# Kernel optimization log

Measured on AMD Instinct MI355X. Metric: run time of the kernel, lower is better.

The kernel has to match this reference:

```python
import jax, jax.numpy as jnp
import numpy as np

K = 4                 # max_block_size (depthwise conv kernel size)
BLOCKS = (1, 2, 3, 4) # block sizes, offset 0
DS = 4                # downsample_factor
BLOCK_MULT = 12       # lcm(1,2,3,4)
DIM = 512
NUM_TOKENS = 256


def setup_inputs() -> dict:
    key = jax.random.key(0)
    ks = jax.random.split(key, 8)
    b, n = 4, 4096
    s = 0.02
    return {
        "x": jax.random.randint(ks[0], (b, n), 0, NUM_TOKENS),
        "emb": jax.random.normal(ks[1], (NUM_TOKENS, DIM), dtype=jnp.float32) * s,
        "conv_w": jax.random.normal(ks[2], (DIM, K), dtype=jnp.float32) * s,   # depthwise Conv1d weight [d,1,K] squeezed
        "conv_b": jax.random.normal(ks[3], (DIM,), dtype=jnp.float32) * s,
        "proj_w": jax.random.normal(ks[4], (DIM, DIM), dtype=jnp.float32) * s,  # 1x1 conv == linear [out,in]
        "proj_b": jax.random.normal(ks[5], (DIM,), dtype=jnp.float32) * s,
        "score_w": jax.random.normal(ks[6], (DIM,), dtype=jnp.float32) * s,     # nn.Linear(dim,1)
        "score_b": jax.random.normal(ks[7], (), dtype=jnp.float32) * s,
    }


def reference(x, emb, conv_w, conv_b, proj_w, proj_b, score_w, score_b):
    b, n = x.shape
    h = emb[x]  # [b, n, d] token embedding (gather)

    # pos_conv: pad (K-1) at sequence end, depthwise conv (valid), then pointwise proj
    hp = jnp.pad(h, ((0, 0), (0, K - 1), (0, 0)))
    y = conv_b + sum(hp[:, k:k + n, :] * conv_w[:, k] for k in range(K))  # [b, n, d]
    h = y @ proj_w.T + proj_b

    # pad sequence to multiple of lcm of block sizes
    L = -(-n // BLOCK_MULT) * BLOCK_MULT
    h = jnp.pad(h, ((0, 0), (0, L - n), (0, 0)))

    # multi-scale block mean pooling, upsampled back to length L
    reprs = []
    for bs in BLOCKS:
        r = h.reshape(b, L // bs, bs, DIM).mean(axis=2)     # [b, L/bs, d]
        reprs.append(jnp.repeat(r, bs, axis=1))             # [b, L, d]
    block_reprs = jnp.stack(reprs, axis=2)                  # [b, L, nb, d]

    # per-position block scores
    scores = block_reprs @ score_w + score_b                # [b, L, nb]
    scores = jax.nn.softmax(scores, axis=2)

    # consensus attention over positions (d = nb = len(BLOCKS))
    sim = jnp.einsum('bid,bjd->bij', scores, scores)        # [b, L, L]
    attn = jax.nn.softmax(sim, axis=-1)
    scores = jnp.einsum('bij,bjm->bim', attn, scores)       # [b, L, nb]

    # fuse block representations and downsample
    out = jnp.einsum('bnkd,bnk->bnd', block_reprs, scores)  # [b, L, d]
    m = -(-n // DS) * DS                                    # == n (4096 divisible by 4)
    out = out[:, :m].reshape(b, m // DS, DS, DIM).mean(axis=2)
    return out
```

## Files before the change

### kernel.cpp

```cpp
#include <hip/hip_runtime.h>
#include <hip/hip_bf16.h>

#define B_ 4
#define N_ 4096
#define L_ 4104
#define D_ 512
#define BK 64
#define NF 210
#define ZCH 36
#define ZCHUNKS 114

typedef __attribute__((ext_vector_type(8))) short bf16x8;
typedef __attribute__((ext_vector_type(4))) float f32x4;

__global__ __launch_bounds__(256) void k_g(const float* __restrict__ emb,
    const float* __restrict__ pw, const float* __restrict__ cwp,
    const float* __restrict__ cb, const float* __restrict__ pb,
    const float* __restrict__ sw,
    float* __restrict__ G, float* __restrict__ biasp,
    unsigned* __restrict__ featPk, float* __restrict__ featCf,
    float* __restrict__ Zg, float* __restrict__ TS, float* __restrict__ c0g) {
  __shared__ __align__(16) __hip_bfloat16 As[2][64 * BK];
  __shared__ __align__(16) __hip_bfloat16 Bs[2][128 * BK];
  __shared__ __align__(16) float cwS[512];
  __shared__ float red[4];
  __shared__ __align__(16) float swS[512];
  __shared__ __align__(16) float uS[512];
  __shared__ __align__(16) float vkS[512];
  const int bx = blockIdx.x;
  const int t = threadIdx.x;
  const int w = t >> 6, l = t & 63;

  if (bx >= 129) {
    const int kp = bx - 129;
    swS[t] = sw[t]; swS[t + 256] = sw[t + 256];
    __syncthreads();
    const int c2 = t * 2;
    float ux0 = 0.f, uy0 = 0.f, ux1 = 0.f, uy1 = 0.f;
#pragma unroll 4
    for (int o = 0; o < 512; o += 2) {
      const float s0 = swS[o], s1 = swS[o + 1];
      const float2 w0 = *(const float2*)(pw + (size_t)o * 512 + c2);
      const float2 w1 = *(const float2*)(pw + (size_t)(o + 1) * 512 + c2);
      ux0 += s0 * w0.x; uy0 += s0 * w0.y;
      ux1 += s1 * w1.x; uy1 += s1 * w1.y;
    }
    const float ux = ux0 + ux1, uy = uy0 + uy1;
    uS[c2] = ux; uS[c2 + 1] = uy;
    vkS[c2]     = ux * cwp[c2 * 4 + kp];
    vkS[c2 + 1] = uy * cwp[(c2 + 1) * 4 + kp];
    __syncthreads();
    const int r16 = t & 15, tg = t >> 4;
    for (int tok0 = 0; tok0 < 256; tok0 += 16) {
      const int tok = tok0 + tg;
      float dot = 0.f;
#pragma unroll
      for (int it = 0; it < 8; ++it) {
        const int c = it * 64 + r16 * 4;
        const float4 e4 = *(const float4*)(emb + (size_t)tok * 512 + c);
        const float4 v4 = *(const float4*)(vkS + c);
        dot += e4.x * v4.x + e4.y * v4.y + e4.z * v4.z + e4.w * v4.w;
      }
#pragma unroll
      for (int m = 8; m >= 1; m >>= 1) dot += __shfl_xor(dot, m);
      if (r16 == 0) TS[kp * 256 + tok] = dot;
    }
    if (kp == 0) {
      float part = cb[c2] * uS[c2] + cb[c2 + 1] * uS[c2 + 1]
                 + pb[c2] * swS[c2] + pb[c2 + 1] * swS[c2 + 1];
#pragma unroll
      for (int m = 32; m >= 1; m >>= 1) part += __shfl_xor(part, m);
      if (l == 0) red[w] = part;
      __syncthreads();
      if (t == 0) c0g[0] = red[0] + red[1] + red[2] + red[3];
    }
    return;
  }
  if (bx == 128) {
    for (int zi = t; zi < B_ * NF * 5; zi += 256) Zg[zi] = 0.f;
    if (t < NF) {
      int idx = 0, mp = 0, mq = 0, mr = 0, ms = 0;
      for (int m = 0; m <= 6; ++m)
        for (int p = m; p >= 0; --p)
          for (int q = m - p; q >= 0; --q)
            for (int r = m - p - q; r >= 0; --r) {
              const int s4 = m - p - q - r;
              if (idx == t) { mp = p; mq = q; mr = r; ms = s4; }
              ++idx;
            }
      featPk[t] = (unsigned)mp | ((unsigned)mq << 8) | ((unsigned)mr << 16) | ((unsigned)ms << 24);
      const float invf[7] = {1.f, 1.f, 0.5f, 1.f/6.f, 1.f/24.f, 1.f/120.f, 1.f/720.f};
      featCf[t] = invf[mp] * invf[mq] * invf[mr] * invf[ms];
    }
    return;
  }
  if (bx >= 64) {
    const int o0 = (bx - 64) * 8;
    const float2 cv = *(const float2*)(cb + t * 2);
#pragma unroll
    for (int oo = 0; oo < 8; ++oo) {
      const int o = o0 + oo;
      const float2 wv = *(const float2*)(pw + (size_t)o * 512 + t * 2);
      float s = wv.x * cv.x + wv.y * cv.y;
#pragma unroll
      for (int off = 32; off > 0; off >>= 1) s += __shfl_xor(s, off);
      if (l == 0) red[w] = s;
      __syncthreads();
      if (t == 0) biasp[o] = red[0] + red[1] + red[2] + red[3] + pb[o];
      __syncthreads();
    }
    return;
  }

  const int m0 = (bx & 3) * 64;
  const int n0 = ((bx >> 2) & 3) * 128;
  const int kp = bx >> 4;
  const int quad = l >> 4, r16 = l & 15;
  const int wc = w * 32;

  cwS[t]       = cwp[t * 4 + kp];
  cwS[t + 256] = cwp[(t + 256) * 4 + kp];

  f32x4 acc[4][2];
#pragma unroll
  for (int a = 0; a < 4; ++a)
#pragma unroll
    for (int bq = 0; bq < 2; ++bq) acc[a][bq] = (f32x4){0.f, 0.f, 0.f, 0.f};

  const int ra = t >> 2, ga0 = (t & 3) * 2;
  const int rb = t >> 1, gb0 = (t & 1) * 4;

#define STAGEG(buf, kb)                                                          \
  _Pragma("unroll")                                                              \
  for (int gi = 0; gi < 2; ++gi) {                                               \
    const int g = ga0 + gi;                                                      \
    const int c0 = (kb) + g * 8;                                                 \
    const float4 a0 = *(const float4*)(emb + (size_t)(m0 + ra) * 512 + c0);      \
    const float4 a1 = *(const float4*)(emb + (size_t)(m0 + ra) * 512 + c0 + 4);  \
    const float4 w0 = *(const float4*)(cwS + c0);                                \
    const float4 w1 = *(const float4*)(cwS + c0 + 4);                            \
    union { __hip_bfloat16 q[8]; bf16x8 v; } ua;                                 \
    ua.q[0] = __float2bfloat16(a0.x * w0.x); ua.q[1] = __float2bfloat16(a0.y * w0.y); \
    ua.q[2] = __float2bfloat16(a0.z * w0.z); ua.q[3] = __float2bfloat16(a0.w * w0.w); \
    ua.q[4] = __float2bfloat16(a1.x * w1.x); ua.q[5] = __float2bfloat16(a1.y * w1.y); \
    ua.q[6] = __float2bfloat16(a1.z * w1.z); ua.q[7] = __float2bfloat16(a1.w * w1.w); \
    *(bf16x8*)(&As[buf][ra * BK + ((g ^ (ra & 7)) * 8)]) = ua.v;                 \
  }                                                                              \
  _Pragma("unroll")                                                              \
  for (int gi = 0; gi < 4; ++gi) {                                               \
    const int g = gb0 + gi;                                                      \
    const int c0 = (kb) + g * 8;                                                 \
    const float4 b0 = *(const float4*)(pw + (size_t)(n0 + rb) * 512 + c0);       \
    const float4 b1 = *(const float4*)(pw + (size_t)(n0 + rb) * 512 + c0 + 4);   \
    union { __hip_bfloat16 q[8]; bf16x8 v; } ub;                                 \
    ub.q[0] = __float2bfloat16(b0.x); ub.q[1] = __float2bfloat16(b0.y);          \
    ub.q[2] = __float2bfloat16(b0.z); ub.q[3] = __float2bfloat16(b0.w);          \
    ub.q[4] = __float2bfloat16(b1.x); ub.q[5] = __float2bfloat16(b1.y);          \
    ub.q[6] = __float2bfloat16(b1.z); ub.q[7] = __float2bfloat16(b1.w);          \
    *(bf16x8*)(&Bs[buf][rb * BK + ((g ^ (rb & 7)) * 8)]) = ub.v;                 \
  }

  __syncthreads();
  STAGEG(0, 0)
  __syncthreads();

#pragma unroll 1
  for (int kt = 0; kt < 8; ++kt) {
    const int cur = kt & 1;
    if (kt < 7) { STAGEG(1 - cur, (kt + 1) * BK) }
#pragma unroll
    for (int kk = 0; kk < 2; ++kk) {
      const int col_e = (kk * 32 + quad * 8) ^ ((r16 & 7) * 8);
      bf16x8 af[4], bfr[2];
#pragma unroll
      for (int ti = 0; ti < 4; ++ti)
        af[ti] = *(const bf16x8*)(&As[cur][(ti * 16 + r16) * BK + col_e]);
#pragma unroll
      for (int tj = 0; tj < 2; ++tj)
        bfr[tj] = *(const bf16x8*)(&Bs[cur][(wc + tj * 16 + r16) * BK + col_e]);
#pragma unroll
      for (int ti = 0; ti < 4; ++ti)
#pragma unroll
        for (int tj = 0; tj < 2; ++tj)
          acc[ti][tj] = __builtin_amdgcn_mfma_f32_16x16x32_bf16(af[ti], bfr[tj], acc[ti][tj], 0, 0, 0);
    }
    __syncthreads();
  }
#undef STAGEG

#pragma unroll
  for (int ti = 0; ti < 4; ++ti) {
    const int gi0 = m0 + ti * 16 + quad * 4;
#pragma unroll
    for (int tj = 0; tj < 2; ++tj) {
      const int go = n0 + wc + tj * 16 + r16;
#pragma unroll
      for (int r = 0; r < 4; ++r)
        G[((size_t)kp * 256 + gi0 + r) * 512 + go] = acc[ti][tj][r];
    }
  }
}

__device__ __forceinline__ float4 softmax4(const float* __restrict__ tw, int base,
                                           int i, float bb) {
  const float s0 = tw[i - base] + bb;
  const int j2 = i & ~1;
  const float s1 = (tw[j2 - base] + tw[j2 + 1 - base]) * 0.5f + bb;
  const int j3 = (i / 3) * 3;
  const float s2 = (tw[j3 - base] + tw[j3 + 1 - base] + tw[j3 + 2 - base]) * (1.f / 3.f) + bb;
  const int j4 = i & ~3;
  const float s3 = (tw[j4 - base] + tw[j4 + 1 - base] + tw[j4 + 2 - base] + tw[j4 + 3 - base]) * 0.25f + bb;
  const float m = fmaxf(fmaxf(s0, s1), fmaxf(s2, s3));
  const float e0 = __expf(s0 - m), e1 = __expf(s1 - m), e2 = __expf(s2 - m), e3 = __expf(s3 - m);
  const float inv = 1.f / (e0 + e1 + e2 + e3);
  return make_float4(e0 * inv, e1 * inv, e2 * inv, e3 * inv);
}

__global__ __launch_bounds__(256) void k_zphi(const int* __restrict__ x,
    const float* __restrict__ TS, const float* __restrict__ c0g,
    const float* __restrict__ sb, const unsigned* __restrict__ featPk,
    float* __restrict__ Zg) {
  __shared__ float twj[ZCH];
  __shared__ float P[ZCH][32];
  __shared__ unsigned pkS[NF];
  const int bx = blockIdx.x;
  const int b = bx / ZCHUNKS, jc = bx % ZCHUNKS;
  const int t = threadIdx.x;
  const int j0 = jc * ZCH;
  if (t < NF) pkS[t] = featPk[t];
  if (t < ZCH) {
    const int j = j0 + t;
    float tv = 0.f;
    if (j < N_) {
      tv = c0g[0];
      const int* xb = x + b * N_;
#pragma unroll
      for (int k = 0; k < 4; ++k)
        if (j + k < N_) tv += TS[k * 256 + xb[j + k]];
    }
    twj[t] = tv;
  }
  __syncthreads();
  const float bb = sb[0];
  if (t < ZCH) {
    const float4 s = softmax4(twj, j0, j0 + t, bb);
    float* p = &P[t][0];
    float va = 1.f, vb = 1.f, vc = 1.f, vd = 1.f;
    p[0] = 1.f; p[8] = 1.f; p[16] = 1.f; p[24] = 1.f;
#pragma unroll
    for (int e = 1; e < 8; ++e) {
      va *= s.x; vb *= s.y; vc *= s.z; vd *= s.w;
      p[e] = va; p[8 + e] = vb; p[16 + e] = vc; p[24 + e] = vd;
    }
  }
  __syncthreads();
  if (t < NF) {
    const unsigned pk = pkS[t];
    const int p = pk & 255, q = (pk >> 8) & 255, r = (pk >> 16) & 255, s4 = pk >> 24;
    float z0 = 0.f, z1 = 0.f, z2 = 0.f, z3 = 0.f, z4 = 0.f;
#pragma unroll 2
    for (int jj = 0; jj < ZCH; ++jj) {
      const float* pp = &P[jj][0];
      const float pa0 = pp[p],       pa1 = pp[p + 1];
      const float pb0 = pp[8 + q],   pb1 = pp[8 + q + 1];
      const float pc0 = pp[16 + r],  pc1 = pp[16 + r + 1];
      const float pd0 = pp[24 + s4], pd1 = pp[24 + s4 + 1];
      const float cd = pc0 * pd0, ab = pa0 * pb0;
      z4 += pa0 * (pb0 * cd);
      z0 += pa1 * (pb0 * cd);
      z1 += pb1 * (pa0 * cd);
      z2 += pc1 * (ab * pd0);
      z3 += pd1 * (ab * pc0);
    }
    float* zb = Zg + (size_t)(b * NF + t) * 5;
    atomicAdd(zb + 0, z0); atomicAdd(zb + 1, z1); atomicAdd(zb + 2, z2);
    atomicAdd(zb + 3, z3); atomicAdd(zb + 4, z4);
  }
}

__global__ __launch_bounds__(256) void k_fuse(const int* __restrict__ x,
    const float* __restrict__ G, const float* __restrict__ biasp,
    const float* __restrict__ TS, const float* __restrict__ c0g,
    const float* __restrict__ sb, const unsigned* __restrict__ featPk,
    const float* __restrict__ featCf, const float* __restrict__ Zg,
    float* __restrict__ out) {
  __shared__ __align__(16) float4 wgtS[12];
  __shared__ float tbS[12];
  __shared__ float Pr[12][32];
  __shared__ float Zl[NF * 5];
  __shared__ unsigned pkS[NF];
  __shared__ float cfS[NF];
  __shared__ int tokS[16];
  const int bx = blockIdx.x;
  const int b = bx / 342, j12 = bx % 342;
  const int t = threadIdx.x, d = t * 2;
  const int r0 = 12 * j12;

  if (t < NF) { pkS[t] = featPk[t]; cfS[t] = featCf[t]; }
  for (int i2 = t; i2 < NF * 5; i2 += 256) Zl[i2] = Zg[(size_t)b * NF * 5 + i2];
  if (t < 15) {
    const int j = r0 + t;
    tokS[t] = (j < N_) ? x[b * N_ + j] : -1;
  }
  __syncthreads();

  const float2 bp = *(const float2*)(biasp + d);
  float2 hv[12];
#pragma unroll
  for (int q = 0; q < 12; ++q) {
    float2 a = make_float2(0.f, 0.f);
    if (r0 + q < N_) {
      a = bp;
#pragma unroll
      for (int k = 0; k < 4; ++k) {
        const int tk = tokS[q + k];
        if (tk >= 0) {
          const float2 g = *(const float2*)(G + ((size_t)k * 256 + tk) * 512 + d);
          a.x += g.x; a.y += g.y;
        }
      }
    }
    hv[q] = a;
  }

  if (t < 12) {
    const int row = r0 + t;
    float tv = 0.f;
    if (row < N_) {
      tv = c0g[0];
#pragma unroll
      for (int k = 0; k < 4; ++k) {
        const int tk = tokS[t + k];
        if (tk >= 0) tv += TS[k * 256 + tk];
      }
    }
    tbS[t] = tv;
  }
  __syncthreads();
  if (t < 12) {
    const float4 s = softmax4(tbS, r0, r0 + t, sb[0]);
    float* p = &Pr[t][0];
    float va = 1.f, vb = 1.f, vc = 1.f, vd = 1.f;
    p[0] = 1.f; p[8] = 1.f; p[16] = 1.f; p[24] = 1.f;
#pragma unroll
    for (int e = 1; e < 8; ++e) {
      va *= s.x; vb *= s.y; vc *= s.z; vd *= s.w;
      p[e] = va; p[8 + e] = vb; p[16 + e] = vc; p[24 + e] = vd;
    }
  }
  __syncthreads();
  if (t < 192) {
    const int row = t >> 4, fi = t & 15;
    float n0 = 0.f, n1 = 0.f, n2 = 0.f, n3 = 0.f, dn = 0.f;
    const float* pr = &Pr[row][0];
    for (int f = fi; f < NF; f += 16) {
      const unsigned pk = pkS[f];
      const float val = cfS[f] * pr[pk & 255] * pr[8 + ((pk >> 8) & 255)]
                                * pr[16 + ((pk >> 16) & 255)] * pr[24 + (pk >> 24)];
      const float* z = &Zl[f * 5];
      n0 += val * z[0]; n1 += val * z[1]; n2 += val * z[2]; n3 += val * z[3];
      dn += val * z[4];
    }
#pragma unroll
    for (int m = 8; m >= 1; m >>= 1) {
      n0 += __shfl_xor(n0, m); n1 += __shfl_xor(n1, m); n2 += __shfl_xor(n2, m);
      n3 += __shfl_xor(n3, m); dn += __shfl_xor(dn, m);
    }
    if (fi == 0) {
      const float inv = 1.f / dn;
      wgtS[row] = make_float4(n0 * inv, n1 * inv, n2 * inv, n3 * inv);
    }
  }
  __syncthreads();

  float2 p2[6], p3[4], p4[3];
#pragma unroll
  for (int g = 0; g < 6; ++g) {
    p2[g].x = (hv[2 * g].x + hv[2 * g + 1].x) * 0.5f;
    p2[g].y = (hv[2 * g].y + hv[2 * g + 1].y) * 0.5f;
  }
#pragma unroll
  for (int g = 0; g < 4; ++g) {
    p3[g].x = (hv[3 * g].x + hv[3 * g + 1].x + hv[3 * g + 2].x) * (1.f / 3.f);
    p3[g].y = (hv[3 * g].y + hv[3 * g + 1].y + hv[3 * g + 2].y) * (1.f / 3.f);
  }
#pragma unroll
  for (int g = 0; g < 3; ++g) {
    p4[g].x = (hv[4 * g].x + hv[4 * g + 1].x + hv[4 * g + 2].x + hv[4 * g + 3].x) * 0.25f;
    p4[g].y = (hv[4 * g].y + hv[4 * g + 1].y + hv[4 * g + 2].y + hv[4 * g + 3].y) * 0.25f;
  }

#pragma unroll
  for (int o = 0; o < 3; ++o) {
    const int orow = j12 * 3 + o;
    if (orow < 1024) {
      float ox = 0.f, oy = 0.f;
#pragma unroll
      for (int rr = 0; rr < 4; ++rr) {
        const int r = 4 * o + rr;
        const float4 wv = wgtS[r];
        const float2 p1 = hv[r];
        const float2 q2 = p2[r >> 1];
        const float2 q3 = p3[r / 3];
        const float2 q4 = p4[o];
        ox += wv.x * p1.x + wv.y * q2.x + wv.z * q3.x + wv.w * q4.x;
        oy += wv.x * p1.y + wv.y * q2.y + wv.z * q3.y + wv.w * q4.y;
      }
      float2 ov; ov.x = ox * 0.25f; ov.y = oy * 0.25f;
      *(float2*)(out + (size_t)(b * 1024 + orow) * D_ + d) = ov;
    }
  }
}

extern "C" void kernel_launch(void* const* d_in, const int* in_sizes, int n_in,
                              void* d_out, int out_size, void* d_ws, size_t ws_size,
                              hipStream_t stream) {
  const int*   x       = (const int*)d_in[0];
  const float* emb     = (const float*)d_in[1];
  const float* conv_w  = (const float*)d_in[2];
  const float* conv_b  = (const float*)d_in[3];
  const float* proj_w  = (const float*)d_in[4];
  const float* proj_b  = (const float*)d_in[5];
  const float* score_w = (const float*)d_in[6];
  const float* score_b = (const float*)d_in[7];
  float* out = (float*)d_out;

  char* ws = (char*)d_ws;
  size_t off = 0;
  float*    G      = (float*)(ws + off); off += (size_t)4 * 256 * 512 * 4;
  float*    bias   = (float*)(ws + off); off += (size_t)512 * 4;
  float*    Zg     = (float*)(ws + off); off += (size_t)B_ * NF * 5 * 4;
  unsigned* featPk = (unsigned*)(ws + off); off += (size_t)1024;
  float*    featCf = (float*)(ws + off); off += (size_t)1024;
  float*    TS     = (float*)(ws + off); off += (size_t)4 * 256 * 4;
  float*    c0     = (float*)(ws + off); off += (size_t)16;
  (void)in_sizes; (void)n_in; (void)out_size; (void)ws_size;

  k_g<<<133, 256, 0, stream>>>(emb, proj_w, conv_w, conv_b, proj_b, score_w,
                               G, bias, featPk, featCf, Zg, TS, c0);
  k_zphi<<<B_ * ZCHUNKS, 256, 0, stream>>>(x, TS, c0, score_b, featPk, Zg);
  k_fuse<<<B_ * 342, 256, 0, stream>>>(x, G, bias, TS, c0, score_b, featPk, featCf, Zg, out);
}
```

Measured before the change: 150.0 us.

## Derive block scores from G rows instead of precomputed token score tables

Removes the four extra blocks in k_g that precomputed per-token, per-tap score tables (TS) and the constant c0 through a 512x512 matvec. Scores are now recomputed in k_zphi and k_fuse as dot products of the gathered G rows plus bias with score_w, using wave shuffles and a shared-memory reduction. This shortens the k_g critical path, where the four TS blocks each streamed the full projection matrix. In exchange, k_zphi gathers G rows for every position, which adds global traffic and reduction barriers. The scores may also differ slightly because G is computed through a bf16 GEMM.

```diff
diff --git a/kernel.cpp b/kernel.cpp
--- a/kernel.cpp
+++ b/kernel.cpp
@@ -16,66 +16,17 @@
 __global__ __launch_bounds__(256) void k_g(const float* __restrict__ emb,
     const float* __restrict__ pw, const float* __restrict__ cwp,
     const float* __restrict__ cb, const float* __restrict__ pb,
-    const float* __restrict__ sw,
     float* __restrict__ G, float* __restrict__ biasp,
     unsigned* __restrict__ featPk, float* __restrict__ featCf,
-    float* __restrict__ Zg, float* __restrict__ TS, float* __restrict__ c0g) {
+    float* __restrict__ Zg) {
   __shared__ __align__(16) __hip_bfloat16 As[2][64 * BK];
   __shared__ __align__(16) __hip_bfloat16 Bs[2][128 * BK];
   __shared__ __align__(16) float cwS[512];
   __shared__ float red[4];
-  __shared__ __align__(16) float swS[512];
-  __shared__ __align__(16) float uS[512];
-  __shared__ __align__(16) float vkS[512];
   const int bx = blockIdx.x;
   const int t = threadIdx.x;
   const int w = t >> 6, l = t & 63;
 
-  if (bx >= 129) {
-    const int kp = bx - 129;
-    swS[t] = sw[t]; swS[t + 256] = sw[t + 256];
-    __syncthreads();
-    const int c2 = t * 2;
-    float ux0 = 0.f, uy0 = 0.f, ux1 = 0.f, uy1 = 0.f;
-#pragma unroll 4
-    for (int o = 0; o < 512; o += 2) {
-      const float s0 = swS[o], s1 = swS[o + 1];
-      const float2 w0 = *(const float2*)(pw + (size_t)o * 512 + c2);
-      const float2 w1 = *(const float2*)(pw + (size_t)(o + 1) * 512 + c2);
-      ux0 += s0 * w0.x; uy0 += s0 * w0.y;
-      ux1 += s1 * w1.x; uy1 += s1 * w1.y;
-    }
-    const float ux = ux0 + ux1, uy = uy0 + uy1;
-    uS[c2] = ux; uS[c2 + 1] = uy;
-    vkS[c2]     = ux * cwp[c2 * 4 + kp];
-    vkS[c2 + 1] = uy * cwp[(c2 + 1) * 4 + kp];
-    __syncthreads();
-    const int r16 = t & 15, tg = t >> 4;
-    for (int tok0 = 0; tok0 < 256; tok0 += 16) {
-      const int tok = tok0 + tg;
-      float dot = 0.f;
-#pragma unroll
-      for (int it = 0; it < 8; ++it) {
-        const int c = it * 64 + r16 * 4;
-        const float4 e4 = *(const float4*)(emb + (size_t)tok * 512 + c);
-        const float4 v4 = *(const float4*)(vkS + c);
-        dot += e4.x * v4.x + e4.y * v4.y + e4.z * v4.z + e4.w * v4.w;
-      }
-#pragma unroll
-      for (int m = 8; m >= 1; m >>= 1) dot += __shfl_xor(dot, m);
-      if (r16 == 0) TS[kp * 256 + tok] = dot;
-    }
-    if (kp == 0) {
-      float part = cb[c2] * uS[c2] + cb[c2 + 1] * uS[c2 + 1]
-                 + pb[c2] * swS[c2] + pb[c2 + 1] * swS[c2 + 1];
-#pragma unroll
-      for (int m = 32; m >= 1; m >>= 1) part += __shfl_xor(part, m);
-      if (l == 0) red[w] = part;
-      __syncthreads();
-      if (t == 0) c0g[0] = red[0] + red[1] + red[2] + red[3];
-    }
-    return;
-  }
   if (bx == 128) {
     for (int zi = t; zi < B_ * NF * 5; zi += 256) Zg[zi] = 0.f;
     if (t < NF) {
@@ -217,29 +168,47 @@
 }
 
 __global__ __launch_bounds__(256) void k_zphi(const int* __restrict__ x,
-    const float* __restrict__ TS, const float* __restrict__ c0g,
-    const float* __restrict__ sb, const unsigned* __restrict__ featPk,
-    float* __restrict__ Zg) {
+    const float* __restrict__ G, const float* __restrict__ biasp,
+    const float* __restrict__ sw, const float* __restrict__ sb,
+    const unsigned* __restrict__ featPk, float* __restrict__ Zg) {
   __shared__ float twj[ZCH];
   __shared__ float P[ZCH][32];
   __shared__ unsigned pkS[NF];
+  __shared__ int tokS[ZCH + 3];
+  __shared__ float rpart[ZCH][4];
   const int bx = blockIdx.x;
   const int b = bx / ZCHUNKS, jc = bx % ZCHUNKS;
-  const int t = threadIdx.x;
+  const int t = threadIdx.x, d = t * 2, w = t >> 6, l = t & 63;
   const int j0 = jc * ZCH;
   if (t < NF) pkS[t] = featPk[t];
-  if (t < ZCH) {
+  if (t < ZCH + 3) {
     const int j = j0 + t;
-    float tv = 0.f;
-    if (j < N_) {
-      tv = c0g[0];
-      const int* xb = x + b * N_;
-#pragma unroll
-      for (int k = 0; k < 4; ++k)
-        if (j + k < N_) tv += TS[k * 256 + xb[j + k]];
-    }
-    twj[t] = tv;
-  }
+    tokS[t] = (j < N_) ? x[b * N_ + j] : -1;
+  }
+  __syncthreads();
+  const float2 swv = *(const float2*)(sw + d);
+  const float2 bp  = *(const float2*)(biasp + d);
+  const float cpart = bp.x * swv.x + bp.y * swv.y;
+#pragma unroll 2
+  for (int jj = 0; jj < ZCH; ++jj) {
+    float s = 0.f;
+    if (j0 + jj < N_) {
+      s = cpart;
+#pragma unroll
+      for (int k = 0; k < 4; ++k) {
+        const int tk = tokS[jj + k];
+        if (tk >= 0) {
+          const float2 g = *(const float2*)(G + ((size_t)k * 256 + tk) * 512 + d);
+          s += g.x * swv.x + g.y * swv.y;
+        }
+      }
+    }
+#pragma unroll
+    for (int off = 32; off > 0; off >>= 1) s += __shfl_xor(s, off);
+    if (l == 0) rpart[jj][w] = s;
+  }
+  __syncthreads();
+  if (t < ZCH) twj[t] = rpart[t][0] + rpart[t][1] + rpart[t][2] + rpart[t][3];
   __syncthreads();
   const float bb = sb[0];
   if (t < ZCH) {
@@ -280,10 +249,9 @@
 
 __global__ __launch_bounds__(256) void k_fuse(const int* __restrict__ x,
     const float* __restrict__ G, const float* __restrict__ biasp,
-    const float* __restrict__ TS, const float* __restrict__ c0g,
-    const float* __restrict__ sb, const unsigned* __restrict__ featPk,
-    const float* __restrict__ featCf, const float* __restrict__ Zg,
-    float* __restrict__ out) {
+    const float* __restrict__ sw, const float* __restrict__ sb,
+    const unsigned* __restrict__ featPk, const float* __restrict__ featCf,
+    const float* __restrict__ Zg, float* __restrict__ out) {
   __shared__ __align__(16) float4 wgtS[12];
   __shared__ float tbS[12];
   __shared__ float Pr[12][32];
@@ -291,9 +259,10 @@
   __shared__ unsigned pkS[NF];
   __shared__ float cfS[NF];
   __shared__ int tokS[16];
+  __shared__ float tpart[12][4];
   const int bx = blockIdx.x;
   const int b = bx / 342, j12 = bx % 342;
-  const int t = threadIdx.x, d = t * 2;
+  const int t = threadIdx.x, d = t * 2, w = t >> 6, l = t & 63;
   const int r0 = 12 * j12;
 
   if (t < NF) { pkS[t] = featPk[t]; cfS[t] = featCf[t]; }
@@ -304,7 +273,8 @@
   }
   __syncthreads();
 
-  const float2 bp = *(const float2*)(biasp + d);
+  const float2 bp  = *(const float2*)(biasp + d);
+  const float2 swv = *(const float2*)(sw + d);
   float2 hv[12];
 #pragma unroll
   for (int q = 0; q < 12; ++q) {
@@ -322,20 +292,15 @@
     }
     hv[q] = a;
   }
-
-  if (t < 12) {
-    const int row = r0 + t;
-    float tv = 0.f;
-    if (row < N_) {
-      tv = c0g[0];
-#pragma unroll
-      for (int k = 0; k < 4; ++k) {
-        const int tk = tokS[t + k];
-        if (tk >= 0) tv += TS[k * 256 + tk];
-      }
-    }
-    tbS[t] = tv;
-  }
+#pragma unroll
+  for (int q = 0; q < 12; ++q) {
+    float s = hv[q].x * swv.x + hv[q].y * swv.y;
+#pragma unroll
+    for (int off = 32; off > 0; off >>= 1) s += __shfl_xor(s, off);
+    if (l == 0) tpart[q][w] = s;
+  }
+  __syncthreads();
+  if (t < 12) tbS[t] = tpart[t][0] + tpart[t][1] + tpart[t][2] + tpart[t][3];
   __syncthreads();
   if (t < 12) {
     const float4 s = softmax4(tbS, r0, r0 + t, sb[0]);
@@ -432,12 +397,9 @@
   float*    Zg     = (float*)(ws + off); off += (size_t)B_ * NF * 5 * 4;
   unsigned* featPk = (unsigned*)(ws + off); off += (size_t)1024;
   float*    featCf = (float*)(ws + off); off += (size_t)1024;
-  float*    TS     = (float*)(ws + off); off += (size_t)4 * 256 * 4;
-  float*    c0     = (float*)(ws + off); off += (size_t)16;
   (void)in_sizes; (void)n_in; (void)out_size; (void)ws_size;
 
-  k_g<<<133, 256, 0, stream>>>(emb, proj_w, conv_w, conv_b, proj_b, score_w,
-                               G, bias, featPk, featCf, Zg, TS, c0);
-  k_zphi<<<B_ * ZCHUNKS, 256, 0, stream>>>(x, TS, c0, score_b, featPk, Zg);
-  k_fuse<<<B_ * 342, 256, 0, stream>>>(x, G, bias, TS, c0, score_b, featPk, featCf, Zg, out);
+  k_g<<<129, 256, 0, stream>>>(emb, proj_w, conv_w, conv_b, proj_b, G, bias, featPk, featCf, Zg);
+  k_zphi<<<B_ * ZCHUNKS, 256, 0, stream>>>(x, G, bias, score_w, score_b, featPk, Zg);
+  k_fuse<<<B_ * 342, 256, 0, stream>>>(x, G, bias, score_w, score_b, featPk, featCf, Zg, out);
 }
```

Result: slower. 168.0 us (+12.0%).

## Compute token scores from G in a separate kernel and transpose P layout

Applied to the files above, without the earlier changes.

Removes the four extra blocks in k_g that recomputed score_w·proj_w and embedding dot products from scratch. A new small kernel k_ts instead derives TS by dotting the already computed G rows with score_w, and c0 from bias·score_w. k_zphi stores the power table transposed with padding, stages tokens in shared memory and unrolls its loop further, and k_fuse pads its power table. This adds a kernel launch and a dependency on G being finished, while cutting redundant full-size reads of proj_w and emb.

```diff
diff --git a/kernel.cpp b/kernel.cpp
--- a/kernel.cpp
+++ b/kernel.cpp
@@ -9,6 +9,7 @@
 #define NF 210
 #define ZCH 36
 #define ZCHUNKS 114
+#define PST 37
 
 typedef __attribute__((ext_vector_type(8))) short bf16x8;
 typedef __attribute__((ext_vector_type(4))) float f32x4;
@@ -16,66 +17,17 @@
 __global__ __launch_bounds__(256) void k_g(const float* __restrict__ emb,
     const float* __restrict__ pw, const float* __restrict__ cwp,
     const float* __restrict__ cb, const float* __restrict__ pb,
-    const float* __restrict__ sw,
     float* __restrict__ G, float* __restrict__ biasp,
     unsigned* __restrict__ featPk, float* __restrict__ featCf,
-    float* __restrict__ Zg, float* __restrict__ TS, float* __restrict__ c0g) {
+    float* __restrict__ Zg) {
   __shared__ __align__(16) __hip_bfloat16 As[2][64 * BK];
   __shared__ __align__(16) __hip_bfloat16 Bs[2][128 * BK];
   __shared__ __align__(16) float cwS[512];
   __shared__ float red[4];
-  __shared__ __align__(16) float swS[512];
-  __shared__ __align__(16) float uS[512];
-  __shared__ __align__(16) float vkS[512];
   const int bx = blockIdx.x;
   const int t = threadIdx.x;
   const int w = t >> 6, l = t & 63;
 
-  if (bx >= 129) {
-    const int kp = bx - 129;
-    swS[t] = sw[t]; swS[t + 256] = sw[t + 256];
-    __syncthreads();
-    const int c2 = t * 2;
-    float ux0 = 0.f, uy0 = 0.f, ux1 = 0.f, uy1 = 0.f;
-#pragma unroll 4
-    for (int o = 0; o < 512; o += 2) {
-      const float s0 = swS[o], s1 = swS[o + 1];
-      const float2 w0 = *(const float2*)(pw + (size_t)o * 512 + c2);
-      const float2 w1 = *(const float2*)(pw + (size_t)(o + 1) * 512 + c2);
-      ux0 += s0 * w0.x; uy0 += s0 * w0.y;
-      ux1 += s1 * w1.x; uy1 += s1 * w1.y;
-    }
-    const float ux = ux0 + ux1, uy = uy0 + uy1;
-    uS[c2] = ux; uS[c2 + 1] = uy;
-    vkS[c2]     = ux * cwp[c2 * 4 + kp];
-    vkS[c2 + 1] = uy * cwp[(c2 + 1) * 4 + kp];
-    __syncthreads();
-    const int r16 = t & 15, tg = t >> 4;
-    for (int tok0 = 0; tok0 < 256; tok0 += 16) {
-      const int tok = tok0 + tg;
-      float dot = 0.f;
-#pragma unroll
-      for (int it = 0; it < 8; ++it) {
-        const int c = it * 64 + r16 * 4;
-        const float4 e4 = *(const float4*)(emb + (size_t)tok * 512 + c);
-        const float4 v4 = *(const float4*)(vkS + c);
-        dot += e4.x * v4.x + e4.y * v4.y + e4.z * v4.z + e4.w * v4.w;
-      }
-#pragma unroll
-      for (int m = 8; m >= 1; m >>= 1) dot += __shfl_xor(dot, m);
-      if (r16 == 0) TS[kp * 256 + tok] = dot;
-    }
-    if (kp == 0) {
-      float part = cb[c2] * uS[c2] + cb[c2 + 1] * uS[c2 + 1]
-                 + pb[c2] * swS[c2] + pb[c2 + 1] * swS[c2 + 1];
-#pragma unroll
-      for (int m = 32; m >= 1; m >>= 1) part += __shfl_xor(part, m);
-      if (l == 0) red[w] = part;
-      __syncthreads();
-      if (t == 0) c0g[0] = red[0] + red[1] + red[2] + red[3];
-    }
-    return;
-  }
   if (bx == 128) {
     for (int zi = t; zi < B_ * NF * 5; zi += 256) Zg[zi] = 0.f;
     if (t < NF) {
@@ -201,6 +153,38 @@
   }
 }
 
+__global__ __launch_bounds__(256) void k_ts(const float* __restrict__ G,
+    const float* __restrict__ biasp, const float* __restrict__ sw,
+    float* __restrict__ TS, float* __restrict__ c0g) {
+  __shared__ float red[4];
+  const int bx = blockIdx.x;
+  const int t = threadIdx.x, w = t >> 6, l = t & 63;
+  if (bx == 128) {
+    const float2 a = *(const float2*)(biasp + t * 2);
+    const float2 b = *(const float2*)(sw + t * 2);
+    float s = a.x * b.x + a.y * b.y;
+#pragma unroll
+    for (int off = 32; off > 0; off >>= 1) s += __shfl_xor(s, off);
+    if (l == 0) red[w] = s;
+    __syncthreads();
+    if (t == 0) c0g[0] = red[0] + red[1] + red[2] + red[3];
+    return;
+  }
+  const float4 s0 = *(const float4*)(sw + l * 8);
+  const float4 s1 = *(const float4*)(sw + l * 8 + 4);
+#pragma unroll
+  for (int rr = 0; rr < 2; ++rr) {
+    const int row = bx * 8 + w * 2 + rr;
+    const float4 g0 = *(const float4*)(G + (size_t)row * 512 + l * 8);
+    const float4 g1 = *(const float4*)(G + (size_t)row * 512 + l * 8 + 4);
+    float s = g0.x * s0.x + g0.y * s0.y + g0.z * s0.z + g0.w * s0.w
+            + g1.x * s1.x + g1.y * s1.y + g1.z * s1.z + g1.w * s1.w;
+#pragma unroll
+    for (int off = 32; off > 0; off >>= 1) s += __shfl_xor(s, off);
+    if (l == 0) TS[row] = s;
+  }
+}
+
 __device__ __forceinline__ float4 softmax4(const float* __restrict__ tw, int base,
                                            int i, float bb) {
   const float s0 = tw[i - base] + bb;
@@ -221,22 +205,28 @@
     const float* __restrict__ sb, const unsigned* __restrict__ featPk,
     float* __restrict__ Zg) {
   __shared__ float twj[ZCH];
-  __shared__ float P[ZCH][32];
+  __shared__ float P[32][PST];
   __shared__ unsigned pkS[NF];
+  __shared__ int tokS[ZCH + 3];
   const int bx = blockIdx.x;
   const int b = bx / ZCHUNKS, jc = bx % ZCHUNKS;
   const int t = threadIdx.x;
   const int j0 = jc * ZCH;
   if (t < NF) pkS[t] = featPk[t];
+  if (t < ZCH + 3) {
+    const int j = j0 + t;
+    tokS[t] = (j < N_) ? x[b * N_ + j] : -1;
+  }
+  __syncthreads();
   if (t < ZCH) {
-    const int j = j0 + t;
     float tv = 0.f;
-    if (j < N_) {
+    if (j0 + t < N_) {
       tv = c0g[0];
-      const int* xb = x + b * N_;
-#pragma unroll
-      for (int k = 0; k < 4; ++k)
-        if (j + k < N_) tv += TS[k * 256 + xb[j + k]];
+#pragma unroll
+      for (int k = 0; k < 4; ++k) {
+        const int tk = tokS[t + k];
+        if (tk >= 0) tv += TS[k * 256 + tk];
+      }
     }
     twj[t] = tv;
   }
@@ -244,27 +234,29 @@
   const float bb = sb[0];
   if (t < ZCH) {
     const float4 s = softmax4(twj, j0, j0 + t, bb);
-    float* p = &P[t][0];
+    P[0][t] = 1.f; P[8][t] = 1.f; P[16][t] = 1.f; P[24][t] = 1.f;
     float va = 1.f, vb = 1.f, vc = 1.f, vd = 1.f;
-    p[0] = 1.f; p[8] = 1.f; p[16] = 1.f; p[24] = 1.f;
 #pragma unroll
     for (int e = 1; e < 8; ++e) {
       va *= s.x; vb *= s.y; vc *= s.z; vd *= s.w;
-      p[e] = va; p[8 + e] = vb; p[16 + e] = vc; p[24 + e] = vd;
+      P[e][t] = va; P[8 + e][t] = vb; P[16 + e][t] = vc; P[24 + e][t] = vd;
     }
   }
   __syncthreads();
   if (t < NF) {
     const unsigned pk = pkS[t];
     const int p = pk & 255, q = (pk >> 8) & 255, r = (pk >> 16) & 255, s4 = pk >> 24;
+    const float* Ra0 = &P[p][0];       const float* Ra1 = &P[p + 1][0];
+    const float* Rb0 = &P[8 + q][0];   const float* Rb1 = &P[8 + q + 1][0];
+    const float* Rc0 = &P[16 + r][0];  const float* Rc1 = &P[16 + r + 1][0];
+    const float* Rd0 = &P[24 + s4][0]; const float* Rd1 = &P[24 + s4 + 1][0];
     float z0 = 0.f, z1 = 0.f, z2 = 0.f, z3 = 0.f, z4 = 0.f;
-#pragma unroll 2
+#pragma unroll 4
     for (int jj = 0; jj < ZCH; ++jj) {
-      const float* pp = &P[jj][0];
-      const float pa0 = pp[p],       pa1 = pp[p + 1];
-      const float pb0 = pp[8 + q],   pb1 = pp[8 + q + 1];
-      const float pc0 = pp[16 + r],  pc1 = pp[16 + r + 1];
-      const float pd0 = pp[24 + s4], pd1 = pp[24 + s4 + 1];
+      const float pa0 = Ra0[jj], pa1 = Ra1[jj];
+      const float pb0 = Rb0[jj], pb1 = Rb1[jj];
+      const float pc0 = Rc0[jj], pc1 = Rc1[jj];
+      const float pd0 = Rd0[jj], pd1 = Rd1[jj];
       const float cd = pc0 * pd0, ab = pa0 * pb0;
       z4 += pa0 * (pb0 * cd);
       z0 += pa1 * (pb0 * cd);
@@ -286,7 +278,7 @@
     float* __restrict__ out) {
   __shared__ __align__(16) float4 wgtS[12];
   __shared__ float tbS[12];
-  __shared__ float Pr[12][32];
+  __shared__ float Pr[12][33];
   __shared__ float Zl[NF * 5];
   __shared__ unsigned pkS[NF];
   __shared__ float cfS[NF];
@@ -324,9 +316,8 @@
   }
 
   if (t < 12) {
-    const int row = r0 + t;
     float tv = 0.f;
-    if (row < N_) {
+    if (r0 + t < N_) {
       tv = c0g[0];
 #pragma unroll
       for (int k = 0; k < 4; ++k) {
@@ -432,12 +423,12 @@
   float*    Zg     = (float*)(ws + off); off += (size_t)B_ * NF * 5 * 4;
   unsigned* featPk = (unsigned*)(ws + off); off += (size_t)1024;
   float*    featCf = (float*)(ws + off); off += (size_t)1024;
-  float*    TS     = (float*)(ws + off); off += (size_t)4 * 256 * 4;
+  float*    TS     = (float*)(ws + off); off += (size_t)1024 * 4;
   float*    c0     = (float*)(ws + off); off += (size_t)16;
   (void)in_sizes; (void)n_in; (void)out_size; (void)ws_size;
 
-  k_g<<<133, 256, 0, stream>>>(emb, proj_w, conv_w, conv_b, proj_b, score_w,
-                               G, bias, featPk, featCf, Zg, TS, c0);
+  k_g<<<129, 256, 0, stream>>>(emb, proj_w, conv_w, conv_b, proj_b, G, bias, featPk, featCf, Zg);
+  k_ts<<<129, 256, 0, stream>>>(G, bias, score_w, TS, c0);
   k_zphi<<<B_ * ZCHUNKS, 256, 0, stream>>>(x, TS, c0, score_b, featPk, Zg);
   k_fuse<<<B_ * 342, 256, 0, stream>>>(x, G, bias, TS, c0, score_b, featPk, featCf, Zg, out);
 }
```

After: 137.1 us. 8.6% less time.
